# Performance work log

Measured on AMD Instinct MI355X. Metric: run time of the kernel, lower is better.

Reference implementation:

```python
import jax, jax.numpy as jnp
import numpy as np

HIDDEN = 1024
LAYERS = 8
LETTERS = 100
INTER = 16


def setup_inputs() -> dict:
    key = jax.random.key(0)
    ks = jax.random.split(key, 12)
    s_i = 1.0 / np.sqrt(HIDDEN)
    website = jax.random.uniform(ks[0], (1, 2048, LETTERS), dtype=jnp.float32)
    payload = jax.random.uniform(ks[1], (1, 2048, LETTERS), dtype=jnp.float32)
    # stacked LSTMCell params: all cells take the raw input (input_size=LETTERS)
    W_ih = jax.random.uniform(ks[2], (LAYERS, 4 * HIDDEN, LETTERS), jnp.float32, -s_i, s_i)
    W_hh = jax.random.uniform(ks[3], (LAYERS, 4 * HIDDEN, HIDDEN), jnp.float32, -s_i, s_i)
    b_ih = jax.random.uniform(ks[4], (LAYERS, 4 * HIDDEN), jnp.float32, -s_i, s_i)
    b_hh = jax.random.uniform(ks[5], (LAYERS, 4 * HIDDEN), jnp.float32, -s_i, s_i)
    W_lin = jax.random.uniform(ks[6], (INTER, HIDDEN), jnp.float32, -s_i, s_i)
    b_lin = jax.random.uniform(ks[7], (INTER,), jnp.float32, -s_i, s_i)
    s_o = 1.0 / np.sqrt(INTER)
    W_out = jax.random.uniform(ks[8], (1, INTER), jnp.float32, -s_o, s_o)
    b_out = jax.random.uniform(ks[9], (1,), jnp.float32, -s_o, s_o)
    return {"website": website, "payload": payload, "W_ih": W_ih, "W_hh": W_hh,
            "b_ih": b_ih, "b_hh": b_hh, "W_lin": W_lin, "b_lin": b_lin,
            "W_out": W_out, "b_out": b_out}


def _lstm_cell(xt, h, c, Wi, Wh, bi, bh):
    # gates: [4H] = Wi @ xt + Wh @ h + biases (batch==1, stored as vectors)
    g = Wi @ xt + bi + Wh @ h + bh
    i, f, gg, o = jnp.split(g, 4)
    i = jax.nn.sigmoid(i)
    f = jax.nn.sigmoid(f)
    gg = jnp.tanh(gg)
    o = jax.nn.sigmoid(o)
    c2 = f * c + i * gg
    h2 = o * jnp.tanh(c2)
    return h2, c2


def _encoder(x, W_ih, W_hh, b_ih, b_hh, W_lin, b_lin):
    # x: [T, LETTERS] (batch 1 squeezed). One shared (h, c) threaded through
    # both the layer stack and time, exactly like the original code.
    H = W_hh.shape[-1]

    def step(carry, xt):
        def layer(carry, p):
            h, c = carry
            Wi, Wh, bi, bh = p
            return _lstm_cell(xt, h, c, Wi, Wh, bi, bh), None
        carry, _ = jax.lax.scan(layer, carry, (W_ih, W_hh, b_ih, b_hh))
        return carry, None

    init = (jnp.zeros((H,), x.dtype), jnp.zeros((H,), x.dtype))
    (h, c), _ = jax.lax.scan(step, init, x)
    # original applies the Linear to 'output' which is the CELL state c
    return W_lin @ c + b_lin  # [INTER]


def reference(website, payload, W_ih, W_hh, b_ih, b_hh, W_lin, b_lin, W_out, b_out):
    x = jnp.concatenate([website, payload], axis=1)[0]  # [T, LETTERS]
    feat = _encoder(x, W_ih, W_hh, b_ih, b_hh, W_lin, b_lin)  # [INTER]
    out = jax.nn.sigmoid(W_out @ feat + b_out)  # [1]
    return out.reshape(1, 1, 1)
```

## Files before the change

### kernel.cpp

```cpp
#include <hip/hip_runtime.h>
#include <stdint.h>

#define HID 1024
#define NLAYERS 8
#define NLET 100
#define T_TOTAL 4096

typedef uint32_t u32x4 __attribute__((ext_vector_type(4)));

__device__ __forceinline__ uint32_t f2bf(float f) {
    uint32_t u = __float_as_uint(f);
    return (u + 0x7FFFu + ((u >> 16) & 1u)) >> 16;
}
__device__ __forceinline__ float bflo(uint32_t p) { return __uint_as_float(p << 16); }
__device__ __forceinline__ float bfhi(uint32_t p) { return __uint_as_float(p & 0xFFFF0000u); }
__device__ __forceinline__ float sigm(float x) { return 1.0f / (1.0f + __expf(-x)); }
__device__ __forceinline__ float tanh_f(float x) {
    float xx = fminf(fmaxf(x, -15.0f), 15.0f);
    float e = __expf(2.0f * xx);
    return (e - 1.0f) / (e + 1.0f);
}

__device__ __forceinline__ void store_coh_x4(void* p, u32x4 d) {
    asm volatile("global_store_dwordx4 %0, %1, off sc0 sc1" ::"v"(p), "v"(d) : "memory");
}
__device__ __forceinline__ void load_coh_2x4(const void* p0, const void* p1, u32x4& a, u32x4& b) {
    asm volatile(
        "global_load_dwordx4 %0, %2, off sc0 sc1\n\t"
        "global_load_dwordx4 %1, %3, off sc0 sc1\n\t"
        "s_waitcnt vmcnt(0)"
        : "=v"(a), "=v"(b)
        : "v"(p0), "v"(p1)
        : "memory");
}

__global__ void __launch_bounds__(256, 1)
lstm_persistent(const float* __restrict__ website, const float* __restrict__ payload,
                const float* __restrict__ W_ih, const float* __restrict__ W_hh,
                const float* __restrict__ b_ih, const float* __restrict__ b_hh,
                char* mail, float* c_out, int ncopies) {
    __shared__ float h_lds[HID];
    __shared__ float h_new[4];

    const int tid = threadIdx.x;
    const int b = blockIdx.x;
    const int u = tid >> 6;
    const int lane = tid & 63;
    const int k = b * 4 + u;
    const int rcopy = b & (ncopies - 1);

    uint32_t wh[NLAYERS][4][8];
    uint32_t wx[NLAYERS][4];
    float bias[NLAYERS][4];
#pragma unroll
    for (int l = 0; l < NLAYERS; ++l) {
#pragma unroll
        for (int g = 0; g < 4; ++g) {
            const int row = 1024 * g + k;
            const float* src = W_hh + ((size_t)(l * 4096 + row)) * 1024;
#pragma unroll
            for (int p = 0; p < 8; ++p) {
                const int c0 = 2 * lane + 128 * p;
                wh[l][g][p] = f2bf(src[c0]) | (f2bf(src[c0 + 1]) << 16);
            }
            if (lane < 50) {
                const float* sx = W_ih + ((size_t)(l * 4096 + row)) * NLET + 2 * lane;
                wx[l][g] = f2bf(sx[0]) | (f2bf(sx[1]) << 16);
            } else {
                wx[l][g] = 0u;
            }
            bias[l][g] = b_ih[l * 4096 + row] + b_hh[l * 4096 + row];
        }
    }

    ((float4*)h_lds)[tid] = make_float4(0.f, 0.f, 0.f, 0.f);
    float c = 0.0f;
    __syncthreads();

    for (int t = 0; t < T_TOTAL; ++t) {
        float x0 = 0.f, x1 = 0.f;
        if (lane < 50) {
            const float* xp = (t < 2048) ? (website + (size_t)t * NLET)
                                         : (payload + (size_t)(t - 2048) * NLET);
            x0 = xp[2 * lane];
            x1 = xp[2 * lane + 1];
        }
#pragma unroll
        for (int l = 0; l < NLAYERS; ++l) {
            const int s = t * NLAYERS + l + 1;
            const int par = s & 1;

            float2 hv[8];
#pragma unroll
            for (int p = 0; p < 8; ++p)
                hv[p] = *(const float2*)&h_lds[2 * lane + 128 * p];
            float acc0 = 0.f, acc1 = 0.f, acc2 = 0.f, acc3 = 0.f;
#pragma unroll
            for (int p = 0; p < 8; ++p) {
                const float hA = hv[p].x, hB = hv[p].y;
                uint32_t w;
                w = wh[l][0][p]; acc0 = fmaf(bflo(w), hA, acc0); acc0 = fmaf(bfhi(w), hB, acc0);
                w = wh[l][1][p]; acc1 = fmaf(bflo(w), hA, acc1); acc1 = fmaf(bfhi(w), hB, acc1);
                w = wh[l][2][p]; acc2 = fmaf(bflo(w), hA, acc2); acc2 = fmaf(bfhi(w), hB, acc2);
                w = wh[l][3][p]; acc3 = fmaf(bflo(w), hA, acc3); acc3 = fmaf(bfhi(w), hB, acc3);
            }
            {
                uint32_t w;
                w = wx[l][0]; acc0 = fmaf(bflo(w), x0, acc0); acc0 = fmaf(bfhi(w), x1, acc0);
                w = wx[l][1]; acc1 = fmaf(bflo(w), x0, acc1); acc1 = fmaf(bfhi(w), x1, acc1);
                w = wx[l][2]; acc2 = fmaf(bflo(w), x0, acc2); acc2 = fmaf(bfhi(w), x1, acc2);
                w = wx[l][3]; acc3 = fmaf(bflo(w), x0, acc3); acc3 = fmaf(bfhi(w), x1, acc3);
            }
#pragma unroll
            for (int mm = 32; mm > 0; mm >>= 1) {
                acc0 += __shfl_xor(acc0, mm, 64);
                acc1 += __shfl_xor(acc1, mm, 64);
                acc2 += __shfl_xor(acc2, mm, 64);
                acc3 += __shfl_xor(acc3, mm, 64);
            }
            const float gi = sigm(acc0 + bias[l][0]);
            const float gf = sigm(acc1 + bias[l][1]);
            const float gg = tanh_f(acc2 + bias[l][2]);
            const float go = sigm(acc3 + bias[l][3]);
            c = fmaf(gf, c, gi * gg);
            const float hn = go * tanh_f(c);
            if (lane == 0) h_new[u] = hn;
            __syncthreads();

            const float f0 = h_new[0], f1 = h_new[1], f2 = h_new[2], f3 = h_new[3];
            if (tid < ncopies) {
                char* dst = mail + ((size_t)((tid * 2 + par) * 256 + b)) * 32;
                u32x4 d0, d1;
                d0.x = __float_as_uint(f0); d0.y = (uint32_t)s;
                d0.z = __float_as_uint(f1); d0.w = (uint32_t)s;
                d1.x = __float_as_uint(f2); d1.y = (uint32_t)s;
                d1.z = __float_as_uint(f3); d1.w = (uint32_t)s;
                store_coh_x4(dst, d0);
                store_coh_x4(dst + 16, d1);
            }

            {
                const char* srcp = mail + ((size_t)((rcopy * 2 + par) * 256 + tid)) * 32;
                u32x4 a0, a1;
                for (;;) {
                    load_coh_2x4(srcp, srcp + 16, a0, a1);
                    if (a0.y == (uint32_t)s && a0.w == (uint32_t)s &&
                        a1.y == (uint32_t)s && a1.w == (uint32_t)s)
                        break;
                    __builtin_amdgcn_s_sleep(2);
                }
                h_lds[4 * tid + 0] = __uint_as_float(a0.x);
                h_lds[4 * tid + 1] = __uint_as_float(a0.z);
                h_lds[4 * tid + 2] = __uint_as_float(a1.x);
                h_lds[4 * tid + 3] = __uint_as_float(a1.z);
            }
            __syncthreads();
        }
    }

    if (lane == 0) c_out[k] = c;
}

__global__ void head_kernel(const float* __restrict__ c_out, const float* __restrict__ W_lin,
                            const float* __restrict__ b_lin, const float* __restrict__ W_out,
                            const float* __restrict__ b_out, float* out) {
    const int lane = threadIdx.x;
    float cv[16];
    const float4* cp = (const float4*)(c_out + lane * 16);
#pragma unroll
    for (int q = 0; q < 4; ++q) {
        float4 v = cp[q];
        cv[4 * q + 0] = v.x;
        cv[4 * q + 1] = v.y;
        cv[4 * q + 2] = v.z;
        cv[4 * q + 3] = v.w;
    }
    float fsum = 0.f;
#pragma unroll
    for (int i = 0; i < 16; ++i) {
        const float* w = W_lin + (size_t)i * HID + lane * 16;
        float a = 0.f;
#pragma unroll
        for (int m = 0; m < 16; ++m) a = fmaf(w[m], cv[m], a);
#pragma unroll
        for (int mm = 32; mm > 0; mm >>= 1) a += __shfl_xor(a, mm, 64);
        fsum = fmaf(W_out[i], a + b_lin[i], fsum);
    }
    if (lane == 0) out[0] = sigm(fsum + b_out[0]);
}

extern "C" void kernel_launch(void* const* d_in, const int* in_sizes, int n_in, void* d_out,
                              int out_size, void* d_ws, size_t ws_size, hipStream_t stream) {
    (void)in_sizes; (void)n_in; (void)out_size;
    const float* website = (const float*)d_in[0];
    const float* payload = (const float*)d_in[1];
    const float* W_ih = (const float*)d_in[2];
    const float* W_hh = (const float*)d_in[3];
    const float* b_ih = (const float*)d_in[4];
    const float* b_hh = (const float*)d_in[5];
    const float* W_lin = (const float*)d_in[6];
    const float* b_lin = (const float*)d_in[7];
    const float* W_out = (const float*)d_in[8];
    const float* b_out = (const float*)d_in[9];

    int ncopies = 64;
    while (ncopies > 1 && (size_t)ncopies * 16384 + 4096 > ws_size) ncopies >>= 1;
    char* mail = (char*)d_ws;
    float* c_out = (float*)((char*)d_ws + (size_t)ncopies * 16384);

    hipMemsetAsync(mail, 0, (size_t)ncopies * 16384, stream);
    lstm_persistent<<<256, 256, 0, stream>>>(website, payload, W_ih, W_hh, b_ih, b_hh, mail,
                                             c_out, ncopies);
    head_kernel<<<1, 64, 0, stream>>>(c_out, W_lin, b_lin, W_out, b_out, (float*)d_out);
}
```

Before: 295.9 ms.

## Split layers across two wave halves and redesign mailbox with separate tags

Each block now runs 512 threads, and each half holds the register-resident weights for four of the eight layers, halving per-thread register pressure. The cell state moves to LDS so both halves can share it. The replicated 32-byte tagged mailbox is replaced by a single data array plus 4 replicated tag arrays, with one wave writing data then tags after a waitcnt and one wave polling tags with a wave-wide vote before bulk-loading h. This is meant to cut per-step global traffic and polling cost, at the price of idle waves in the inactive half and a data-then-tag ordering dependency.

After: 345.4 ms. +16.7%, slower.

```diff
diff --git a/kernel.cpp b/kernel.cpp
--- a/kernel.cpp
+++ b/kernel.cpp
@@ -24,36 +24,57 @@
 __device__ __forceinline__ void store_coh_x4(void* p, u32x4 d) {
     asm volatile("global_store_dwordx4 %0, %1, off sc0 sc1" ::"v"(p), "v"(d) : "memory");
 }
-__device__ __forceinline__ void load_coh_2x4(const void* p0, const void* p1, u32x4& a, u32x4& b) {
+__device__ __forceinline__ void store_coh_b32(void* p, uint32_t d) {
+    asm volatile("global_store_dword %0, %1, off sc0 sc1" ::"v"(p), "v"(d) : "memory");
+}
+__device__ __forceinline__ u32x4 load_coh_x4(const void* p) {
+    u32x4 a;
+    asm volatile("global_load_dwordx4 %0, %1, off sc0 sc1\n\ts_waitcnt vmcnt(0)"
+                 : "=v"(a)
+                 : "v"(p)
+                 : "memory");
+    return a;
+}
+__device__ __forceinline__ void load_coh_4x4(const void* p0, const void* p1, const void* p2,
+                                             const void* p3, u32x4& a, u32x4& b, u32x4& c,
+                                             u32x4& d) {
     asm volatile(
-        "global_load_dwordx4 %0, %2, off sc0 sc1\n\t"
-        "global_load_dwordx4 %1, %3, off sc0 sc1\n\t"
+        "global_load_dwordx4 %0, %4, off sc0 sc1\n\t"
+        "global_load_dwordx4 %1, %5, off sc0 sc1\n\t"
+        "global_load_dwordx4 %2, %6, off sc0 sc1\n\t"
+        "global_load_dwordx4 %3, %7, off sc0 sc1\n\t"
         "s_waitcnt vmcnt(0)"
-        : "=v"(a), "=v"(b)
-        : "v"(p0), "v"(p1)
+        : "=v"(a), "=v"(b), "=v"(c), "=v"(d)
+        : "v"(p0), "v"(p1), "v"(p2), "v"(p3)
         : "memory");
 }
 
-__global__ void __launch_bounds__(256, 1)
+__global__ void __launch_bounds__(512, 2)
 lstm_persistent(const float* __restrict__ website, const float* __restrict__ payload,
                 const float* __restrict__ W_ih, const float* __restrict__ W_hh,
                 const float* __restrict__ b_ih, const float* __restrict__ b_hh,
-                char* mail, float* c_out, int ncopies) {
-    __shared__ float h_lds[HID];
+                char* mbox, float* c_out) {
+    __shared__ __align__(16) float h_lds[HID];
     __shared__ float h_new[4];
+    __shared__ float c_lds[4];
 
     const int tid = threadIdx.x;
     const int b = blockIdx.x;
-    const int u = tid >> 6;
+    const int w = tid >> 6;
     const int lane = tid & 63;
+    const int u = w & 3;
+    const int half = w >> 2;
     const int k = b * 4 + u;
-    const int rcopy = b & (ncopies - 1);
-
-    uint32_t wh[NLAYERS][4][8];
-    uint32_t wx[NLAYERS][4];
-    float bias[NLAYERS][4];
-#pragma unroll
-    for (int l = 0; l < NLAYERS; ++l) {
+
+    u32x4* dataP = (u32x4*)mbox;
+    uint32_t* tagP = (uint32_t*)(mbox + 8192);
+
+    uint32_t wh[4][4][8];
+    uint32_t wx[4][4];
+    float bias[4][4];
+#pragma unroll
+    for (int ll = 0; ll < 4; ++ll) {
+        const int l = half * 4 + ll;
 #pragma unroll
         for (int g = 0; g < 4; ++g) {
             const int row = 1024 * g + k;
@@ -61,20 +82,20 @@
 #pragma unroll
             for (int p = 0; p < 8; ++p) {
                 const int c0 = 2 * lane + 128 * p;
-                wh[l][g][p] = f2bf(src[c0]) | (f2bf(src[c0 + 1]) << 16);
+                wh[ll][g][p] = f2bf(src[c0]) | (f2bf(src[c0 + 1]) << 16);
             }
             if (lane < 50) {
                 const float* sx = W_ih + ((size_t)(l * 4096 + row)) * NLET + 2 * lane;
-                wx[l][g] = f2bf(sx[0]) | (f2bf(sx[1]) << 16);
+                wx[ll][g] = f2bf(sx[0]) | (f2bf(sx[1]) << 16);
             } else {
-                wx[l][g] = 0u;
-            }
-            bias[l][g] = b_ih[l * 4096 + row] + b_hh[l * 4096 + row];
+                wx[ll][g] = 0u;
+            }
+            bias[ll][g] = b_ih[l * 4096 + row] + b_hh[l * 4096 + row];
         }
     }
 
-    ((float4*)h_lds)[tid] = make_float4(0.f, 0.f, 0.f, 0.f);
-    float c = 0.0f;
+    if (tid < 256) ((float4*)h_lds)[tid] = make_float4(0.f, 0.f, 0.f, 0.f);
+    if (tid < 4) c_lds[tid] = 0.0f;
     __syncthreads();
 
     for (int t = 0; t < T_TOTAL; ++t) {
@@ -90,75 +111,82 @@
             const int s = t * NLAYERS + l + 1;
             const int par = s & 1;
 
-            float2 hv[8];
-#pragma unroll
-            for (int p = 0; p < 8; ++p)
-                hv[p] = *(const float2*)&h_lds[2 * lane + 128 * p];
-            float acc0 = 0.f, acc1 = 0.f, acc2 = 0.f, acc3 = 0.f;
-#pragma unroll
-            for (int p = 0; p < 8; ++p) {
-                const float hA = hv[p].x, hB = hv[p].y;
-                uint32_t w;
-                w = wh[l][0][p]; acc0 = fmaf(bflo(w), hA, acc0); acc0 = fmaf(bfhi(w), hB, acc0);
-                w = wh[l][1][p]; acc1 = fmaf(bflo(w), hA, acc1); acc1 = fmaf(bfhi(w), hB, acc1);
-                w = wh[l][2][p]; acc2 = fmaf(bflo(w), hA, acc2); acc2 = fmaf(bfhi(w), hB, acc2);
-                w = wh[l][3][p]; acc3 = fmaf(bflo(w), hA, acc3); acc3 = fmaf(bfhi(w), hB, acc3);
-            }
-            {
-                uint32_t w;
-                w = wx[l][0]; acc0 = fmaf(bflo(w), x0, acc0); acc0 = fmaf(bfhi(w), x1, acc0);
-                w = wx[l][1]; acc1 = fmaf(bflo(w), x0, acc1); acc1 = fmaf(bfhi(w), x1, acc1);
-                w = wx[l][2]; acc2 = fmaf(bflo(w), x0, acc2); acc2 = fmaf(bfhi(w), x1, acc2);
-                w = wx[l][3]; acc3 = fmaf(bflo(w), x0, acc3); acc3 = fmaf(bfhi(w), x1, acc3);
-            }
-#pragma unroll
-            for (int mm = 32; mm > 0; mm >>= 1) {
-                acc0 += __shfl_xor(acc0, mm, 64);
-                acc1 += __shfl_xor(acc1, mm, 64);
-                acc2 += __shfl_xor(acc2, mm, 64);
-                acc3 += __shfl_xor(acc3, mm, 64);
-            }
-            const float gi = sigm(acc0 + bias[l][0]);
-            const float gf = sigm(acc1 + bias[l][1]);
-            const float gg = tanh_f(acc2 + bias[l][2]);
-            const float go = sigm(acc3 + bias[l][3]);
-            c = fmaf(gf, c, gi * gg);
-            const float hn = go * tanh_f(c);
-            if (lane == 0) h_new[u] = hn;
+            if ((l >> 2) == half) {
+                const int ll = l & 3;
+                float2 hv[8];
+#pragma unroll
+                for (int p = 0; p < 8; ++p) hv[p] = *(const float2*)&h_lds[2 * lane + 128 * p];
+                float acc0 = 0.f, acc1 = 0.f, acc2 = 0.f, acc3 = 0.f;
+#pragma unroll
+                for (int p = 0; p < 8; ++p) {
+                    const float hA = hv[p].x, hB = hv[p].y;
+                    uint32_t ww;
+                    ww = wh[ll][0][p]; acc0 = fmaf(bflo(ww), hA, acc0); acc0 = fmaf(bfhi(ww), hB, acc0);
+                    ww = wh[ll][1][p]; acc1 = fmaf(bflo(ww), hA, acc1); acc1 = fmaf(bfhi(ww), hB, acc1);
+                    ww = wh[ll][2][p]; acc2 = fmaf(bflo(ww), hA, acc2); acc2 = fmaf(bfhi(ww), hB, acc2);
+                    ww = wh[ll][3][p]; acc3 = fmaf(bflo(ww), hA, acc3); acc3 = fmaf(bfhi(ww), hB, acc3);
+                }
+                {
+                    uint32_t ww;
+                    ww = wx[ll][0]; acc0 = fmaf(bflo(ww), x0, acc0); acc0 = fmaf(bfhi(ww), x1, acc0);
+                    ww = wx[ll][1]; acc1 = fmaf(bflo(ww), x0, acc1); acc1 = fmaf(bfhi(ww), x1, acc1);
+                    ww = wx[ll][2]; acc2 = fmaf(bflo(ww), x0, acc2); acc2 = fmaf(bfhi(ww), x1, acc2);
+                    ww = wx[ll][3]; acc3 = fmaf(bflo(ww), x0, acc3); acc3 = fmaf(bfhi(ww), x1, acc3);
+                }
+#pragma unroll
+                for (int mm = 32; mm > 0; mm >>= 1) {
+                    acc0 += __shfl_xor(acc0, mm, 64);
+                    acc1 += __shfl_xor(acc1, mm, 64);
+                    acc2 += __shfl_xor(acc2, mm, 64);
+                    acc3 += __shfl_xor(acc3, mm, 64);
+                }
+                const float gi = sigm(acc0 + bias[ll][0]);
+                const float gf = sigm(acc1 + bias[ll][1]);
+                const float gg = tanh_f(acc2 + bias[ll][2]);
+                const float go = sigm(acc3 + bias[ll][3]);
+                const float cn = fmaf(gf, c_lds[u], gi * gg);
+                const float hn = go * tanh_f(cn);
+                if (lane == 0) {
+                    c_lds[u] = cn;
+                    h_new[u] = hn;
+                }
+            }
             __syncthreads();
 
-            const float f0 = h_new[0], f1 = h_new[1], f2 = h_new[2], f3 = h_new[3];
-            if (tid < ncopies) {
-                char* dst = mail + ((size_t)((tid * 2 + par) * 256 + b)) * 32;
-                u32x4 d0, d1;
-                d0.x = __float_as_uint(f0); d0.y = (uint32_t)s;
-                d0.z = __float_as_uint(f1); d0.w = (uint32_t)s;
-                d1.x = __float_as_uint(f2); d1.y = (uint32_t)s;
-                d1.z = __float_as_uint(f3); d1.w = (uint32_t)s;
-                store_coh_x4(dst, d0);
-                store_coh_x4(dst + 16, d1);
-            }
-
-            {
-                const char* srcp = mail + ((size_t)((rcopy * 2 + par) * 256 + tid)) * 32;
-                u32x4 a0, a1;
+            if (w == 1) {
+                if (lane == 0) {
+                    u32x4 d;
+                    d.x = __float_as_uint(h_new[0]);
+                    d.y = __float_as_uint(h_new[1]);
+                    d.z = __float_as_uint(h_new[2]);
+                    d.w = __float_as_uint(h_new[3]);
+                    store_coh_x4(&dataP[par * 256 + b], d);
+                }
+                asm volatile("s_waitcnt vmcnt(0)" ::: "memory");
+                if (lane < 4) store_coh_b32(&tagP[(par * 4 + lane) * 256 + b], (uint32_t)s);
+            }
+            if (w == 0) {
+                const uint32_t* tp = &tagP[(par * 4 + (b & 3)) * 256 + lane * 4];
+                const uint32_t su = (uint32_t)s;
                 for (;;) {
-                    load_coh_2x4(srcp, srcp + 16, a0, a1);
-                    if (a0.y == (uint32_t)s && a0.w == (uint32_t)s &&
-                        a1.y == (uint32_t)s && a1.w == (uint32_t)s)
-                        break;
-                    __builtin_amdgcn_s_sleep(2);
-                }
-                h_lds[4 * tid + 0] = __uint_as_float(a0.x);
-                h_lds[4 * tid + 1] = __uint_as_float(a0.z);
-                h_lds[4 * tid + 2] = __uint_as_float(a1.x);
-                h_lds[4 * tid + 3] = __uint_as_float(a1.z);
+                    u32x4 tg = load_coh_x4(tp);
+                    const bool ok = (tg.x == su) & (tg.y == su) & (tg.z == su) & (tg.w == su);
+                    if (__all(ok)) break;
+                }
+                const u32x4* dp = &dataP[par * 256];
+                u32x4 a0, a1, a2, a3;
+                load_coh_4x4(dp + lane, dp + lane + 64, dp + lane + 128, dp + lane + 192, a0, a1,
+                             a2, a3);
+                u32x4* hq = (u32x4*)h_lds;
+                hq[lane] = a0;
+                hq[lane + 64] = a1;
+                hq[lane + 128] = a2;
+                hq[lane + 192] = a3;
             }
             __syncthreads();
         }
     }
-
-    if (lane == 0) c_out[k] = c;
+    if (tid < 4) c_out[b * 4 + tid] = c_lds[tid];
 }
 
 __global__ void head_kernel(const float* __restrict__ c_out, const float* __restrict__ W_lin,
@@ -178,10 +206,10 @@
     float fsum = 0.f;
 #pragma unroll
     for (int i = 0; i < 16; ++i) {
-        const float* w = W_lin + (size_t)i * HID + lane * 16;
+        const float* wr = W_lin + (size_t)i * HID + lane * 16;
         float a = 0.f;
 #pragma unroll
-        for (int m = 0; m < 16; ++m) a = fmaf(w[m], cv[m], a);
+        for (int m = 0; m < 16; ++m) a = fmaf(wr[m], cv[m], a);
 #pragma unroll
         for (int mm = 32; mm > 0; mm >>= 1) a += __shfl_xor(a, mm, 64);
         fsum = fmaf(W_out[i], a + b_lin[i], fsum);
@@ -191,7 +219,7 @@
 
 extern "C" void kernel_launch(void* const* d_in, const int* in_sizes, int n_in, void* d_out,
                               int out_size, void* d_ws, size_t ws_size, hipStream_t stream) {
-    (void)in_sizes; (void)n_in; (void)out_size;
+    (void)in_sizes; (void)n_in; (void)out_size; (void)ws_size;
     const float* website = (const float*)d_in[0];
     const float* payload = (const float*)d_in[1];
     const float* W_ih = (const float*)d_in[2];
@@ -203,13 +231,11 @@
     const float* W_out = (const float*)d_in[8];
     const float* b_out = (const float*)d_in[9];
 
-    int ncopies = 64;
-    while (ncopies > 1 && (size_t)ncopies * 16384 + 4096 > ws_size) ncopies >>= 1;
-    char* mail = (char*)d_ws;
-    float* c_out = (float*)((char*)d_ws + (size_t)ncopies * 16384);
-
-    hipMemsetAsync(mail, 0, (size_t)ncopies * 16384, stream);
-    lstm_persistent<<<256, 256, 0, stream>>>(website, payload, W_ih, W_hh, b_ih, b_hh, mail,
-                                             c_out, ncopies);
+    char* mbox = (char*)d_ws;
+    float* c_out = (float*)((char*)d_ws + 16384);
+
+    hipMemsetAsync(mbox, 0, 16384, stream);
+    lstm_persistent<<<256, 512, 0, stream>>>(website, payload, W_ih, W_hh, b_ih, b_hh, mbox,
+                                             c_out);
     head_kernel<<<1, 64, 0, stream>>>(c_out, W_lin, b_lin, W_out, b_out, (float*)d_out);
 }
```
